# Performance work log

Hardware: AMD Instinct MI355X
Metric: run time of the kernel (lower is better)

## Reference

```python
import jax, jax.numpy as jnp
import numpy as np

B = 4096
IN_DIMS = (3, 32, 32)      # in_numel = 3072
OUT_DIMS = (64, 16, 16)    # out_numel = 16384
IN_NUMEL = int(np.prod(IN_DIMS))
OUT_NUMEL = int(np.prod(OUT_DIMS))


def setup_inputs() -> dict:
    key = jax.random.key(0)
    k1, k2, k3, k4 = jax.random.split(key, 4)
    x = jax.random.normal(k1, (B,) + IN_DIMS, dtype=jnp.float32)
    # Cached composed linear operator (out_numel x in_numel); scale ~1/sqrt(fan_in)
    cached_matrix = jax.random.normal(k2, (OUT_NUMEL, IN_NUMEL), dtype=jnp.float32) / np.sqrt(IN_NUMEL)
    cached_matrix_extra = jax.random.uniform(k3, (1,), dtype=jnp.float32) + 0.5
    cached_tensor_extra = jax.random.normal(k4, (IN_NUMEL, IN_NUMEL), dtype=jnp.float32) / IN_NUMEL
    return {
        "x": x,
        "cached_matrix": cached_matrix,
        "cached_matrix_extra": cached_matrix_extra,
        "cached_tensor_extra": cached_tensor_extra,
    }


def reference(x, cached_matrix, cached_matrix_extra, cached_tensor_extra):
    batches = x.shape[0]
    # input_as_matrix: [in_numel, B]
    X = x.reshape(batches, -1).T
    # input_as_matrix_extra: L2 norm per column -> [1, B]
    X_extra = jnp.linalg.norm(X, ord=2, axis=0, keepdims=True)
    # output_as_matrix = M @ X : [out_numel, B]
    Y = jnp.matmul(cached_matrix, X)
    # output_as_matrix_extra = s * ||x|| + sum((T @ X) * X, axis=0)
    Y_extra = cached_matrix_extra * X_extra + jnp.sum(jnp.matmul(cached_tensor_extra, X) * X, axis=0, keepdims=True)
    Y = Y / Y_extra
    return Y.T.reshape(batches, *OUT_DIMS)
```

## Files before the change

### kernel.cpp

```cpp
#include <hip/hip_runtime.h>
#include <hip/hip_bf16.h>

typedef __attribute__((ext_vector_type(8))) short bf16x8;
typedef __attribute__((ext_vector_type(4))) short bf16x4;
typedef __attribute__((ext_vector_type(4))) float f32x4;

#define DEV __device__ __forceinline__

static constexpr int BATCH = 4096;
static constexpr int KDIM  = 3072;
static constexpr int NOUT  = 16384;

DEV unsigned short f2bf(float f) {
  union { float f; unsigned int u; } v; v.f = f;
  unsigned int u = v.u;
  u += 0x7fffu + ((u >> 16) & 1u);
  return (unsigned short)(u >> 16);
}

__global__ __launch_bounds__(256) void prep_x_kernel(
    const float* __restrict__ x, unsigned short* __restrict__ xbf,
    float* __restrict__ nrm) {
  const int b = blockIdx.x;
  const int t = threadIdx.x;
  const float* row = x + (size_t)b * KDIM;
  unsigned short* orow = xbf + (size_t)b * KDIM;
  float ss = 0.f;
#pragma unroll
  for (int i = 0; i < 3; ++i) {
    const int c = i * 256 + t;
    float4 v = reinterpret_cast<const float4*>(row)[c];
    ss += v.x * v.x + v.y * v.y + v.z * v.z + v.w * v.w;
    bf16x4 o;
    o[0] = (short)f2bf(v.x); o[1] = (short)f2bf(v.y);
    o[2] = (short)f2bf(v.z); o[3] = (short)f2bf(v.w);
    reinterpret_cast<bf16x4*>(orow)[c] = o;
  }
#pragma unroll
  for (int off = 32; off > 0; off >>= 1) ss += __shfl_down(ss, off, 64);
  __shared__ float red[4];
  if ((t & 63) == 0) red[t >> 6] = ss;
  __syncthreads();
  if (t == 0) nrm[b] = sqrtf(red[0] + red[1] + red[2] + red[3]);
}

__global__ __launch_bounds__(256) void cvt_kernel(
    const float* __restrict__ src, unsigned short* __restrict__ dst, size_t n4) {
  size_t i = (size_t)blockIdx.x * blockDim.x + threadIdx.x;
  const size_t stride = (size_t)gridDim.x * blockDim.x;
  for (; i < n4; i += stride) {
    float4 v = reinterpret_cast<const float4*>(src)[i];
    bf16x4 o;
    o[0] = (short)f2bf(v.x); o[1] = (short)f2bf(v.y);
    o[2] = (short)f2bf(v.z); o[3] = (short)f2bf(v.w);
    reinterpret_cast<bf16x4*>(dst)[i] = o;
  }
}

__global__ __launch_bounds__(256) void qform_kernel(
    const unsigned short* __restrict__ A,
    const unsigned short* __restrict__ Bm,
    const float* __restrict__ xf,
    float* __restrict__ partial) {
  __shared__ unsigned short ldsA[128 * 32];
  __shared__ unsigned short ldsB[128 * 32];
  const int t = threadIdx.x;
  const int lane = t & 63;
  const int wv = t >> 6;
  const int wr = wv >> 1, wc = wv & 1;
  const int col0 = blockIdx.x * 128;
  const int row0 = blockIdx.y * 128;

  f32x4 acc[4][4];
#pragma unroll
  for (int i = 0; i < 4; ++i)
#pragma unroll
    for (int j = 0; j < 4; ++j) acc[i][j] = (f32x4){0.f, 0.f, 0.f, 0.f};

  const unsigned short* aBase = A + (size_t)row0 * KDIM;
  const unsigned short* bBase = Bm + (size_t)col0 * KDIM;
  const int ldsoff0 = (t & ~63) * 8;

  for (int k0 = 0; k0 < KDIM; k0 += 32) {
    __syncthreads();
#pragma unroll
    for (int i = 0; i < 2; ++i) {
      const int c = i * 256 + t;
      const unsigned short* ga = aBase + (size_t)(c >> 2) * KDIM + (k0 + (c & 3) * 8);
      const unsigned short* gb = bBase + (size_t)(c >> 2) * KDIM + (k0 + (c & 3) * 8);
      __builtin_amdgcn_global_load_lds(
          (const __attribute__((address_space(1))) unsigned int*)(const void*)ga,
          (__attribute__((address_space(3))) unsigned int*)(void*)(ldsA + i * 2048 + ldsoff0),
          16, 0, 0);
      __builtin_amdgcn_global_load_lds(
          (const __attribute__((address_space(1))) unsigned int*)(const void*)gb,
          (__attribute__((address_space(3))) unsigned int*)(void*)(ldsB + i * 2048 + ldsoff0),
          16, 0, 0);
    }
    __syncthreads();
    bf16x8 af[4], bfr[4];
#pragma unroll
    for (int mi = 0; mi < 4; ++mi)
      af[mi] = *reinterpret_cast<const bf16x8*>(
          &ldsA[(wr * 64 + mi * 16 + (lane & 15)) * 32 + (lane >> 4) * 8]);
#pragma unroll
    for (int ni = 0; ni < 4; ++ni)
      bfr[ni] = *reinterpret_cast<const bf16x8*>(
          &ldsB[(wc * 64 + ni * 16 + (lane & 15)) * 32 + (lane >> 4) * 8]);
#pragma unroll
    for (int mi = 0; mi < 4; ++mi)
#pragma unroll
      for (int ni = 0; ni < 4; ++ni)
        acc[mi][ni] = __builtin_amdgcn_mfma_f32_16x16x32_bf16(af[mi], bfr[ni], acc[mi][ni], 0, 0, 0);
  }

#pragma unroll
  for (int mi = 0; mi < 4; ++mi) {
#pragma unroll
    for (int j = 0; j < 4; ++j) {
      const int b = row0 + wr * 64 + mi * 16 + (lane >> 4) * 4 + j;
      const float* xrow = xf + (size_t)b * KDIM + col0 + wc * 64 + (lane & 15);
      float s = 0.f;
#pragma unroll
      for (int ni = 0; ni < 4; ++ni) s += acc[mi][ni][j] * xrow[ni * 16];
      s += __shfl_xor(s, 1, 64);
      s += __shfl_xor(s, 2, 64);
      s += __shfl_xor(s, 4, 64);
      s += __shfl_xor(s, 8, 64);
      if ((lane & 15) == 0) partial[(size_t)b * 48 + blockIdx.x * 2 + wc] = s;
    }
  }
}

__global__ __launch_bounds__(256) void finalize_ye_kernel(
    const float* __restrict__ nrm, const float* __restrict__ partial,
    const float* __restrict__ sp, float* __restrict__ ye) {
  const int b = blockIdx.x * blockDim.x + threadIdx.x;
  if (b >= BATCH) return;
  float qv = 0.f;
#pragma unroll
  for (int i = 0; i < 48; ++i) qv += partial[(size_t)b * 48 + i];
  ye[b] = sp[0] * nrm[b] + qv;
}

template <bool BBF16>
__global__ __launch_bounds__(256) void main_gemm_kernel(
    const unsigned short* __restrict__ A,
    const unsigned short* __restrict__ Bbf,
    const float* __restrict__ Bf,
    const float* __restrict__ ye,
    float* __restrict__ out) {
  __shared__ unsigned short ldsA[128 * 32];
  __shared__ unsigned short ldsB[128 * 32];
  const int t = threadIdx.x;
  const int lane = t & 63;
  const int wv = t >> 6;
  const int wr = wv >> 1, wc = wv & 1;
  const int col0 = blockIdx.x * 128;
  const int row0 = blockIdx.y * 128;

  f32x4 acc[4][4];
#pragma unroll
  for (int i = 0; i < 4; ++i)
#pragma unroll
    for (int j = 0; j < 4; ++j) acc[i][j] = (f32x4){0.f, 0.f, 0.f, 0.f};

  const unsigned short* aBase = A + (size_t)row0 * KDIM;
  const unsigned short* bBase = BBF16 ? (Bbf + (size_t)col0 * KDIM) : nullptr;
  const float* bfBase = BBF16 ? nullptr : (Bf + (size_t)col0 * KDIM);
  const int ldsoff0 = (t & ~63) * 8;

  for (int k0 = 0; k0 < KDIM; k0 += 32) {
    __syncthreads();
#pragma unroll
    for (int i = 0; i < 2; ++i) {
      const int c = i * 256 + t;
      const unsigned short* ga = aBase + (size_t)(c >> 2) * KDIM + (k0 + (c & 3) * 8);
      __builtin_amdgcn_global_load_lds(
          (const __attribute__((address_space(1))) unsigned int*)(const void*)ga,
          (__attribute__((address_space(3))) unsigned int*)(void*)(ldsA + i * 2048 + ldsoff0),
          16, 0, 0);
    }
    if constexpr (BBF16) {
#pragma unroll
      for (int i = 0; i < 2; ++i) {
        const int c = i * 256 + t;
        const unsigned short* gb = bBase + (size_t)(c >> 2) * KDIM + (k0 + (c & 3) * 8);
        __builtin_amdgcn_global_load_lds(
            (const __attribute__((address_space(1))) unsigned int*)(const void*)gb,
            (__attribute__((address_space(3))) unsigned int*)(void*)(ldsB + i * 2048 + ldsoff0),
            16, 0, 0);
      }
    } else {
#pragma unroll
      for (int i = 0; i < 2; ++i) {
        const int c = i * 256 + t;
        const int r = c >> 1, ko = (c & 1) * 16;
        const float* gp = bfBase + (size_t)r * KDIM + k0 + ko;
        unsigned short tmp[16];
#pragma unroll
        for (int q = 0; q < 4; ++q) {
          float4 v = reinterpret_cast<const float4*>(gp)[q];
          tmp[q * 4 + 0] = f2bf(v.x); tmp[q * 4 + 1] = f2bf(v.y);
          tmp[q * 4 + 2] = f2bf(v.z); tmp[q * 4 + 3] = f2bf(v.w);
        }
#pragma unroll
        for (int q = 0; q < 2; ++q)
          *reinterpret_cast<bf16x8*>(&ldsB[r * 32 + ko + q * 8]) =
              *reinterpret_cast<const bf16x8*>(&tmp[q * 8]);
      }
    }
    __syncthreads();
    bf16x8 af[4], bfr[4];
#pragma unroll
    for (int mi = 0; mi < 4; ++mi)
      af[mi] = *reinterpret_cast<const bf16x8*>(
          &ldsA[(wr * 64 + mi * 16 + (lane & 15)) * 32 + (lane >> 4) * 8]);
#pragma unroll
    for (int ni = 0; ni < 4; ++ni)
      bfr[ni] = *reinterpret_cast<const bf16x8*>(
          &ldsB[(wc * 64 + ni * 16 + (lane & 15)) * 32 + (lane >> 4) * 8]);
#pragma unroll
    for (int mi = 0; mi < 4; ++mi)
#pragma unroll
      for (int ni = 0; ni < 4; ++ni)
        acc[mi][ni] = __builtin_amdgcn_mfma_f32_16x16x32_bf16(af[mi], bfr[ni], acc[mi][ni], 0, 0, 0);
  }

#pragma unroll
  for (int mi = 0; mi < 4; ++mi) {
#pragma unroll
    for (int j = 0; j < 4; ++j) {
      const int b = row0 + wr * 64 + mi * 16 + (lane >> 4) * 4 + j;
      const float r = 1.0f / ye[b];
      float* orow = out + (size_t)b * NOUT + col0 + wc * 64 + (lane & 15);
#pragma unroll
      for (int ni = 0; ni < 4; ++ni) orow[ni * 16] = acc[mi][ni][j] * r;
    }
  }
}

extern "C" void kernel_launch(void* const* d_in, const int* in_sizes, int n_in,
                              void* d_out, int out_size, void* d_ws, size_t ws_size,
                              hipStream_t stream) {
  (void)in_sizes; (void)n_in; (void)out_size;
  const float* x  = (const float*)d_in[0];
  const float* M  = (const float*)d_in[1];
  const float* sc = (const float*)d_in[2];
  const float* T  = (const float*)d_in[3];
  float* out = (float*)d_out;
  char* ws = (char*)d_ws;

  size_t off = 0;
  auto wsalloc = [&](size_t bytes) -> void* {
    void* p = ws + off;
    off += (bytes + 255) & ~(size_t)255;
    return p;
  };
  unsigned short* Xbf = (unsigned short*)wsalloc((size_t)BATCH * KDIM * 2);
  unsigned short* Tbf = (unsigned short*)wsalloc((size_t)KDIM * KDIM * 2);
  float* nrm = (float*)wsalloc((size_t)BATCH * 4);
  float* ye  = (float*)wsalloc((size_t)BATCH * 4);
  float* partial = (float*)wsalloc((size_t)BATCH * 48 * 4);
  unsigned short* Mbf = (unsigned short*)wsalloc((size_t)NOUT * KDIM * 2);
  const bool useMbf = (off <= ws_size);

  prep_x_kernel<<<BATCH, 256, 0, stream>>>(x, Xbf, nrm);
  cvt_kernel<<<1024, 256, 0, stream>>>(T, Tbf, (size_t)KDIM * KDIM / 4);
  if (useMbf)
    cvt_kernel<<<2048, 256, 0, stream>>>(M, Mbf, (size_t)NOUT * KDIM / 4);
  qform_kernel<<<dim3(KDIM / 128, BATCH / 128), 256, 0, stream>>>(Xbf, Tbf, x, partial);
  finalize_ye_kernel<<<BATCH / 256, 256, 0, stream>>>(nrm, partial, sc, ye);
  if (useMbf)
    main_gemm_kernel<true><<<dim3(NOUT / 128, BATCH / 128), 256, 0, stream>>>(
        Xbf, Mbf, nullptr, ye, out);
  else
    main_gemm_kernel<false><<<dim3(NOUT / 128, BATCH / 128), 256, 0, stream>>>(
        Xbf, nullptr, M, ye, out);
}
```

Measured before the change: 684.5 us.

## Replace main bf16 GEMM with 256x256 double-buffered 8-wave pipelined kernel

Adds a new GEMM kernel for the bf16 path. It uses 256x256 output tiles with BK=64 and 512 threads (8 waves). Global-to-LDS loads are double-buffered, the LDS layout is XOR-swizzled, and loads for the next tile are staged in quarter-tile phases interleaved with MFMA work, using explicit vmcnt waits and priority bumps. Workgroup IDs are remapped for better L2 locality. The goal is to hide memory latency and raise data reuse compared with the single-buffered 128x128 kernel. The cost is 128KB of LDS, a large accumulator register footprint, and hand-tuned synchronisation that is fragile.

```diff
diff --git a/kernel.cpp b/kernel.cpp
--- a/kernel.cpp
+++ b/kernel.cpp
@@ -143,10 +143,145 @@
   ye[b] = sp[0] * nrm[b] + qv;
 }
 
-template <bool BBF16>
+static constexpr int BK8 = 64;
+static constexpr int NKT = KDIM / BK8;
+
+#define LDSE(BUF, OP, HALF) ((BUF)*32768 + (OP)*16384 + (HALF)*8192)
+
+#define STAGE8(OP, HALF, S, BUF)                                             \
+  {                                                                          \
+    const unsigned short* gb_ = (OP) ? Bm : A;                               \
+    const int gr0_ = ((OP) ? col0 : row0) + (HALF)*128;                      \
+    _Pragma("unroll")                                                        \
+    for (int j_ = 0; j_ < 2; ++j_) {                                         \
+      const int row_ = j_*64 + wid*8 + (lane >> 3);                          \
+      const int le_  = ((lane & 7)*8) ^ ((row_ & 7) << 3);                   \
+      __builtin_amdgcn_global_load_lds(                                      \
+        (const __attribute__((address_space(1))) unsigned int*)(const void*) \
+          (gb_ + (size_t)(gr0_ + row_)*KDIM + (S)*BK8 + le_),                \
+        (__attribute__((address_space(3))) unsigned int*)(void*)             \
+          (lds + LDSE(BUF, OP, HALF) + j_*4096 + wid*512),                   \
+        16, 0, 0);                                                           \
+    }                                                                        \
+  }
+
+#define LOADFRAGS8(P, QM, QN)                                                \
+  _Pragma("unroll")                                                          \
+  for (int mi = 0; mi < 4; ++mi) {                                           \
+    const int r_ = wm*64 + mi*16 + (lane & 15);                              \
+    const int xv_ = (r_ & 7) << 3;                                           \
+    _Pragma("unroll")                                                        \
+    for (int ks = 0; ks < 2; ++ks)                                           \
+      aft[mi][ks] = *reinterpret_cast<const bf16x8*>(                        \
+          lds + LDSE(P, 0, QM) + ((r_*64 + ks*32 + (lane >> 4)*8) ^ xv_));   \
+  }                                                                          \
+  _Pragma("unroll")                                                          \
+  for (int ni = 0; ni < 2; ++ni) {                                           \
+    const int r_ = wn*32 + ni*16 + (lane & 15);                              \
+    const int xv_ = (r_ & 7) << 3;                                           \
+    _Pragma("unroll")                                                        \
+    for (int ks = 0; ks < 2; ++ks)                                           \
+      bft[ni][ks] = *reinterpret_cast<const bf16x8*>(                        \
+          lds + LDSE(P, 1, QN) + ((r_*64 + ks*32 + (lane >> 4)*8) ^ xv_));   \
+  }
+
+#define MMA8(QM, QN)                                                         \
+  __builtin_amdgcn_s_setprio(1);                                             \
+  _Pragma("unroll")                                                          \
+  for (int mi = 0; mi < 4; ++mi)                                             \
+    _Pragma("unroll")                                                        \
+    for (int ni = 0; ni < 2; ++ni)                                           \
+      _Pragma("unroll")                                                      \
+      for (int ks = 0; ks < 2; ++ks)                                         \
+        acc[(QM)*4 + mi][(QN)*2 + ni] =                                      \
+            __builtin_amdgcn_mfma_f32_16x16x32_bf16(                         \
+                aft[mi][ks], bft[ni][ks], acc[(QM)*4 + mi][(QN)*2 + ni],     \
+                0, 0, 0);                                                    \
+  __builtin_amdgcn_s_setprio(0);
+
+#define VMW(N)                                                               \
+  asm volatile("s_waitcnt vmcnt(" #N ")" ::: "memory");                      \
+  __builtin_amdgcn_sched_barrier(0)
+
+#define NOVM (void)0
+
+#define PHASE8(P, QM, QN, STAGESTMT, VMSTMT)                                 \
+  LOADFRAGS8(P, QM, QN);                                                     \
+  __builtin_amdgcn_s_barrier();                                              \
+  STAGESTMT;                                                                 \
+  MMA8(QM, QN);                                                              \
+  VMSTMT;                                                                    \
+  __builtin_amdgcn_s_barrier();
+
+#define TILE8(P, T)                                                          \
+  PHASE8(P, 0, 0, STAGE8(1, 1, (T) + 1, (P) ^ 1), NOVM);                     \
+  PHASE8(P, 0, 1, STAGE8(0, 0, (T) + 2, P), NOVM);                           \
+  PHASE8(P, 1, 0, STAGE8(1, 0, (T) + 2, P), NOVM);                           \
+  PHASE8(P, 1, 1, STAGE8(0, 1, (T) + 2, P), VMW(6));
+
+__global__ __launch_bounds__(512) void gemm8_kernel(
+    const unsigned short* __restrict__ A,
+    const unsigned short* __restrict__ Bm,
+    const float* __restrict__ ye,
+    float* __restrict__ out) {
+  __shared__ unsigned short lds[65536];
+  const int t = threadIdx.x;
+  const int lane = t & 63, wid = t >> 6;
+  const int wm = wid >> 2, wn = wid & 3;
+
+  const int bid = blockIdx.x;
+  const int wgid = (bid & 7) * 128 + (bid >> 3);
+  const int bx = wgid & 63;
+  const int by = wgid >> 6;
+  const int row0 = by * 256, col0 = bx * 256;
+
+  f32x4 acc[8][4];
+#pragma unroll
+  for (int i = 0; i < 8; ++i)
+#pragma unroll
+    for (int j = 0; j < 4; ++j) acc[i][j] = (f32x4){0.f, 0.f, 0.f, 0.f};
+
+  bf16x8 aft[4][2], bft[2][2];
+
+  STAGE8(0, 0, 0, 0); STAGE8(1, 0, 0, 0); STAGE8(0, 1, 0, 0); STAGE8(1, 1, 0, 0);
+  STAGE8(0, 0, 1, 1); STAGE8(1, 0, 1, 1); STAGE8(0, 1, 1, 1);
+  VMW(6);
+  __builtin_amdgcn_s_barrier();
+
+#pragma unroll 1
+  for (int i = 0; i < 23; ++i) {
+    const int t0 = 2 * i;
+    TILE8(0, t0);
+    TILE8(1, t0 + 1);
+  }
+
+  PHASE8(0, 0, 0, STAGE8(1, 1, 47, 1), NOVM);
+  PHASE8(0, 0, 1, NOVM, NOVM);
+  PHASE8(0, 1, 0, NOVM, NOVM);
+  PHASE8(0, 1, 1, NOVM, VMW(0));
+  PHASE8(1, 0, 0, NOVM, NOVM);
+  PHASE8(1, 0, 1, NOVM, NOVM);
+  PHASE8(1, 1, 0, NOVM, NOVM);
+  PHASE8(1, 1, 1, NOVM, NOVM);
+
+#pragma unroll
+  for (int am = 0; am < 8; ++am) {
+#pragma unroll
+    for (int j = 0; j < 4; ++j) {
+      const int b = row0 + (am >> 2) * 128 + wm * 64 + (am & 3) * 16 +
+                    (lane >> 4) * 4 + j;
+      const float r = 1.0f / ye[b];
+      float* orow = out + (size_t)b * NOUT + col0;
+#pragma unroll
+      for (int an = 0; an < 4; ++an)
+        orow[(an >> 1) * 128 + wn * 32 + (an & 1) * 16 + (lane & 15)] =
+            acc[am][an][j] * r;
+    }
+  }
+}
+
 __global__ __launch_bounds__(256) void main_gemm_kernel(
     const unsigned short* __restrict__ A,
-    const unsigned short* __restrict__ Bbf,
     const float* __restrict__ Bf,
     const float* __restrict__ ye,
     float* __restrict__ out) {
@@ -166,8 +301,7 @@
     for (int j = 0; j < 4; ++j) acc[i][j] = (f32x4){0.f, 0.f, 0.f, 0.f};
 
   const unsigned short* aBase = A + (size_t)row0 * KDIM;
-  const unsigned short* bBase = BBF16 ? (Bbf + (size_t)col0 * KDIM) : nullptr;
-  const float* bfBase = BBF16 ? nullptr : (Bf + (size_t)col0 * KDIM);
+  const float* bfBase = Bf + (size_t)col0 * KDIM;
   const int ldsoff0 = (t & ~63) * 8;
 
   for (int k0 = 0; k0 < KDIM; k0 += 32) {
@@ -181,34 +315,22 @@
           (__attribute__((address_space(3))) unsigned int*)(void*)(ldsA + i * 2048 + ldsoff0),
           16, 0, 0);
     }
-    if constexpr (BBF16) {
-#pragma unroll
-      for (int i = 0; i < 2; ++i) {
-        const int c = i * 256 + t;
-        const unsigned short* gb = bBase + (size_t)(c >> 2) * KDIM + (k0 + (c & 3) * 8);
-        __builtin_amdgcn_global_load_lds(
-            (const __attribute__((address_space(1))) unsigned int*)(const void*)gb,
-            (__attribute__((address_space(3))) unsigned int*)(void*)(ldsB + i * 2048 + ldsoff0),
-            16, 0, 0);
+#pragma unroll
+    for (int i = 0; i < 2; ++i) {
+      const int c = i * 256 + t;
+      const int r = c >> 1, ko = (c & 1) * 16;
+      const float* gp = bfBase + (size_t)r * KDIM + k0 + ko;
+      unsigned short tmp[16];
+#pragma unroll
+      for (int q = 0; q < 4; ++q) {
+        float4 v = reinterpret_cast<const float4*>(gp)[q];
+        tmp[q * 4 + 0] = f2bf(v.x); tmp[q * 4 + 1] = f2bf(v.y);
+        tmp[q * 4 + 2] = f2bf(v.z); tmp[q * 4 + 3] = f2bf(v.w);
       }
-    } else {
-#pragma unroll
-      for (int i = 0; i < 2; ++i) {
-        const int c = i * 256 + t;
-        const int r = c >> 1, ko = (c & 1) * 16;
-        const float* gp = bfBase + (size_t)r * KDIM + k0 + ko;
-        unsigned short tmp[16];
-#pragma unroll
-        for (int q = 0; q < 4; ++q) {
-          float4 v = reinterpret_cast<const float4*>(gp)[q];
-          tmp[q * 4 + 0] = f2bf(v.x); tmp[q * 4 + 1] = f2bf(v.y);
-          tmp[q * 4 + 2] = f2bf(v.z); tmp[q * 4 + 3] = f2bf(v.w);
-        }
-#pragma unroll
-        for (int q = 0; q < 2; ++q)
-          *reinterpret_cast<bf16x8*>(&ldsB[r * 32 + ko + q * 8]) =
-              *reinterpret_cast<const bf16x8*>(&tmp[q * 8]);
-      }
+#pragma unroll
+      for (int q = 0; q < 2; ++q)
+        *reinterpret_cast<bf16x8*>(&ldsB[r * 32 + ko + q * 8]) =
+            *reinterpret_cast<const bf16x8*>(&tmp[q * 8]);
     }
     __syncthreads();
     bf16x8 af[4], bfr[4];
@@ -272,9 +394,9 @@
   qform_kernel<<<dim3(KDIM / 128, BATCH / 128), 256, 0, stream>>>(Xbf, Tbf, x, partial);
   finalize_ye_kernel<<<BATCH / 256, 256, 0, stream>>>(nrm, partial, sc, ye);
   if (useMbf)
-    main_gemm_kernel<true><<<dim3(NOUT / 128, BATCH / 128), 256, 0, stream>>>(
-        Xbf, Mbf, nullptr, ye, out);
+    gemm8_kernel<<<dim3((NOUT / 256) * (BATCH / 256)), 512, 0, stream>>>(
+        Xbf, Mbf, ye, out);
   else
-    main_gemm_kernel<false><<<dim3(NOUT / 128, BATCH / 128), 256, 0, stream>>>(
-        Xbf, nullptr, M, ye, out);
-}
+    main_gemm_kernel<<<dim3(NOUT / 128, BATCH / 128), 256, 0, stream>>>(
+        Xbf, M, ye, out);
+}
```

New measurement: 606.9 us. 1.13x faster.
